# Kernel tuning notes

Hardware: AMD Instinct MI355X
Metric: run time of the kernel (lower is better)

The kernel has to match this reference:

```python
import jax, jax.numpy as jnp
import numpy as np

B, T, F1, F2 = 16384, 5, 300, 251
IN, H = 551, 128

def setup_inputs() -> dict:
    key = jax.random.key(0)
    ks = jax.random.split(key, 16)
    s = 0.05
    return {
        "x1": jax.random.normal(ks[0], (B, T, F1), jnp.float32),
        "x2": jax.random.normal(ks[1], (B, T, F2), jnp.float32),
        "W_ih": jax.random.normal(ks[2], (4 * H, IN), jnp.float32) * s,
        "W_hh": jax.random.normal(ks[3], (4 * H, H), jnp.float32) * s,
        "b_ih": jax.random.normal(ks[4], (4 * H,), jnp.float32) * s,
        "b_hh": jax.random.normal(ks[5], (4 * H,), jnp.float32) * s,
        "W1": jax.random.normal(ks[6], (531, H * T), jnp.float32) * s,
        "b1": jax.random.normal(ks[7], (531,), jnp.float32) * s,
        "W2": jax.random.normal(ks[8], (256, 531), jnp.float32) * s,
        "b2": jax.random.normal(ks[9], (256,), jnp.float32) * s,
        "W3": jax.random.normal(ks[10], (64, 256), jnp.float32) * s,
        "b3": jax.random.normal(ks[11], (64,), jnp.float32) * s,
        "W4": jax.random.normal(ks[12], (2, 64), jnp.float32) * s,
        "b4": jax.random.normal(ks[13], (2,), jnp.float32) * s,
    }

def _lstm(x, W_ih, W_hh, b_ih, b_hh):
    # x: [B, T, IN] -> outputs [B, T, H]; PyTorch gate order i, f, g, o
    xg = jnp.einsum('bti,gi->btg', x, W_ih) + b_ih + b_hh  # [B, T, 4H]
    xg = jnp.transpose(xg, (1, 0, 2))  # [T, B, 4H]
    h0 = jnp.zeros((x.shape[0], H), x.dtype)
    c0 = jnp.zeros((x.shape[0], H), x.dtype)

    def step(carry, xg_t):
        h, c = carry
        g = xg_t + h @ W_hh.T  # [B, 4H]
        i, f, gg, o = jnp.split(g, 4, axis=-1)
        c = jax.nn.sigmoid(f) * c + jax.nn.sigmoid(i) * jnp.tanh(gg)
        h = jax.nn.sigmoid(o) * jnp.tanh(c)
        return (h, c), h

    _, hs = jax.lax.scan(step, (h0, c0), xg)  # hs: [T, B, H]
    return jnp.transpose(hs, (1, 0, 2))

def reference(x1, x2, W_ih, W_hh, b_ih, b_hh, W1, b1, W2, b2, W3, b3, W4, b4):
    x = jnp.concatenate((x1, x2), axis=2)  # [B, T, 551]
    h = _lstm(x, W_ih, W_hh, b_ih, b_hh)   # [B, T, H]
    h = h.reshape(h.shape[0], T * H)
    h = jax.nn.relu(h @ W1.T + b1)
    h = jax.nn.relu(h @ W2.T + b2)
    h = jax.nn.relu(h @ W3.T + b3)
    logits = h @ W4.T + b4
    return jax.nn.softmax(logits, axis=1)
```

## Files before the change

### kernel.cpp

```cpp
#include <hip/hip_runtime.h>
#include <hip/hip_bf16.h>


typedef short  short8  __attribute__((ext_vector_type(8)));
typedef short  short4v __attribute__((ext_vector_type(4)));
typedef float  f32x4   __attribute__((ext_vector_type(4)));

#define MFMA(a, b, c) __builtin_amdgcn_mfma_f32_16x16x32_bf16((a), (b), (c), 0, 0, 0)

__device__ __forceinline__ short f2bs(float f) {
    __hip_bfloat16 h = __float2bfloat16(f);
    union { __hip_bfloat16 h; short s; } u; u.h = h; return u.s;
}
__device__ __forceinline__ float b2f(short s) {
    union { unsigned u; float f; } v; v.u = ((unsigned)(unsigned short)s) << 16; return v.f;
}
__device__ __forceinline__ float sigf(float x)  { return 1.f / (1.f + __expf(-x)); }
__device__ __forceinline__ float mytanh(float x){ return 2.f / (1.f + __expf(-2.f * x)) - 1.f; }

#define BB     16384
#define TT     5
#define F1     300
#define F2     251
#define INF    551
#define KP     576
#define G4     512
#define HH     128
#define FLAT   640
#define L1N    531
#define L1P    576
#define L1KP   544
#define L2N    256
#define L3N    64

#define O_WIH  0u
#define O_WHH  589824u
#define O_W1   720896u
#define O_W2   1458176u
#define O_W3   1736704u
#define O_BG   1769472u
#define O_B1   1771520u
#define O_XG   1773824u
#define O_HS   85659904u
#define WS_NEED 106631424u

__device__ __forceinline__ void pack_b(const float* __restrict__ W, short* __restrict__ dst,
                                       int i, int tpn, int Nsrc, int Ksrc, int ldw)
{
    int tile = i >> 9, rem = i & 511, lane = rem >> 3, jj = rem & 7;
    int tn = tile / tpn, tk = tile - tn * tpn;
    int n = tn * 16 + (lane & 15);
    int k = tk * 32 + (lane >> 4) * 8 + jj;
    float v = (n < Nsrc && k < Ksrc) ? W[n * ldw + k] : 0.f;
    dst[i] = f2bs(v);
}

__global__ void prep_kernel(
    const float* __restrict__ W_ih, const float* __restrict__ W_hh,
    const float* __restrict__ b_ih, const float* __restrict__ b_hh,
    const float* __restrict__ W1,   const float* __restrict__ b1,
    const float* __restrict__ W2,   const float* __restrict__ W3,
    short* __restrict__ Wihp, short* __restrict__ Whhp, float* __restrict__ biasg,
    short* __restrict__ W1p,  float* __restrict__ b1p,  short* __restrict__ W2p,
    short* __restrict__ W3p)
{
    const int N0 = G4 * KP;
    const int N1 = N0 + G4 * HH;
    const int N2 = N1 + L1P * FLAT;
    const int N3 = N2 + L2N * L1KP;
    const int N4 = N3 + L3N * L2N;
    const int N5 = N4 + G4;
    const int N6 = N5 + L1P;
    const int stride = gridDim.x * blockDim.x;
    for (int i = blockIdx.x * blockDim.x + threadIdx.x; i < N6; i += stride) {
        if (i < N0)      pack_b(W_ih, Wihp, i,       18, G4,  INF, INF);
        else if (i < N1) pack_b(W_hh, Whhp, i - N0,   4, G4,  HH,  HH);
        else if (i < N2) pack_b(W1,   W1p,  i - N1,  20, L1N, FLAT, FLAT);
        else if (i < N3) pack_b(W2,   W2p,  i - N2,  17, L2N, L1N, L1N);
        else if (i < N4) pack_b(W3,   W3p,  i - N3,   8, L3N, L2N, L2N);
        else if (i < N5) { int j = i - N4; biasg[j] = b_ih[j] + b_hh[j]; }
        else             { int j = i - N5; b1p[j] = (j < L1N) ? b1[j] : 0.f; }
    }
}

__device__ __forceinline__ float4 ld4(const float* __restrict__ x1r,
                                      const float* __restrict__ x2r, int c)
{
    if (c + 3 < F1) return *(const float4*)(x1r + c);
    if (c + 3 < INF) return *(const float4*)(x2r + (c - F1));
    float4 r;
    r.x = (c + 0 < INF) ? x2r[c - F1 + 0] : 0.f;
    r.y = (c + 1 < INF) ? x2r[c - F1 + 1] : 0.f;
    r.z = (c + 2 < INF) ? x2r[c - F1 + 2] : 0.f;
    r.w = (c + 3 < INF) ? x2r[c - F1 + 3] : 0.f;
    return r;
}

__global__ __launch_bounds__(512, 4) void k1_xgemm(
    const float* __restrict__ x1, const float* __restrict__ x2,
    const short* __restrict__ Wihp, const float* __restrict__ biasg,
    short* __restrict__ xg)
{
    __shared__ __align__(16) short At[2][64][72];
    const int tid  = threadIdx.x;
    const int w    = tid >> 6;
    const int lane = tid & 63;
    const int quad = lane >> 4;
    const int c16  = lane & 15;
    const int m0   = blockIdx.x * 64;
    const int t    = m0 >> 14;
    const int bb   = m0 & 16383;

    const int srow  = tid >> 3;
    const int kslot = tid & 7;
    const float* x1r = x1 + ((size_t)(bb + srow) * TT + t) * F1;
    const float* x2r = x2 + ((size_t)(bb + srow) * TT + t) * F2;

    f32x4 acc[4][4];
#pragma unroll
    for (int mt = 0; mt < 4; ++mt)
#pragma unroll
        for (int nt = 0; nt < 4; ++nt)
            acc[mt][nt] = (f32x4){0.f, 0.f, 0.f, 0.f};

    {
        int c = kslot * 8;
        float4 v0 = *(const float4*)(x1r + c);
        float4 v1 = *(const float4*)(x1r + c + 4);
        short8 s;
        s[0] = f2bs(v0.x); s[1] = f2bs(v0.y); s[2] = f2bs(v0.z); s[3] = f2bs(v0.w);
        s[4] = f2bs(v1.x); s[5] = f2bs(v1.y); s[6] = f2bs(v1.z); s[7] = f2bs(v1.w);
        *(short8*)&At[0][srow][kslot * 8] = s;
    }
    __syncthreads();

    for (int ch = 0; ch < 9; ++ch) {
        const int cur = ch & 1;
        float4 q0, q1;
        if (ch < 8) {
            int c = (ch + 1) * 64 + kslot * 8;
            q0 = ld4(x1r, x2r, c);
            q1 = ld4(x1r, x2r, c + 4);
        }
#pragma unroll
        for (int ks = 0; ks < 2; ++ks) {
            short8 a[4];
#pragma unroll
            for (int mt = 0; mt < 4; ++mt)
                a[mt] = *(const short8*)&At[cur][mt * 16 + c16][ks * 32 + quad * 8];
            const int tk = ch * 2 + ks;
#pragma unroll
            for (int nt = 0; nt < 4; ++nt) {
                short8 b = *(const short8*)&Wihp[(((w * 4 + nt) * 18 + tk) << 9) + lane * 8];
#pragma unroll
                for (int mt = 0; mt < 4; ++mt)
                    acc[mt][nt] = MFMA(a[mt], b, acc[mt][nt]);
            }
        }
        if (ch < 8) {
            short8 s;
            s[0] = f2bs(q0.x); s[1] = f2bs(q0.y); s[2] = f2bs(q0.z); s[3] = f2bs(q0.w);
            s[4] = f2bs(q1.x); s[5] = f2bs(q1.y); s[6] = f2bs(q1.z); s[7] = f2bs(q1.w);
            *(short8*)&At[cur ^ 1][srow][kslot * 8] = s;
        }
        __syncthreads();
    }

#pragma unroll
    for (int nt = 0; nt < 4; ++nt) {
        float bv = biasg[w * 64 + nt * 16 + c16];
#pragma unroll
        for (int mt = 0; mt < 4; ++mt) {
            short4v o;
#pragma unroll
            for (int r = 0; r < 4; ++r) o[r] = f2bs(acc[mt][nt][r] + bv);
            int tm = (m0 >> 4) + mt, tn = w * 4 + nt;
            *(short4v*)&xg[((tm * 32 + tn) << 8) + lane * 4] = o;
        }
    }
}

__global__ __launch_bounds__(512, 2) void k2_rec(
    const short* __restrict__ Whhp, const short* __restrict__ xg,
    short* __restrict__ hs)
{
    __shared__ __align__(16) short hb[2][32][136];
    const int tid  = threadIdx.x;
    const int w    = tid >> 6;
    const int lane = tid & 63;
    const int quad = lane >> 4;
    const int c16  = lane & 15;
    const int btile = blockIdx.x * 2;

    short8 bfr[4][4];
#pragma unroll
    for (int g = 0; g < 4; ++g)
#pragma unroll
        for (int ks = 0; ks < 4; ++ks)
            bfr[g][ks] = *(const short8*)&Whhp[((((g * 8 + w) * 4) + ks) << 9) + lane * 8];

    float cst[2][4];
#pragma unroll
    for (int mt = 0; mt < 2; ++mt)
#pragma unroll
        for (int r = 0; r < 4; ++r) cst[mt][r] = 0.f;

    const int j = w * 16 + c16;

    for (int t = 0; t < TT; ++t) {
        short4v xq[2][4];
#pragma unroll
        for (int mt = 0; mt < 2; ++mt)
#pragma unroll
            for (int g = 0; g < 4; ++g)
                xq[mt][g] = *(const short4v*)
                    &xg[((((t << 10) + btile + mt) * 32 + (g * 8 + w)) << 8) + lane * 4];

        f32x4 acc[2][4];
#pragma unroll
        for (int mt = 0; mt < 2; ++mt)
#pragma unroll
            for (int g = 0; g < 4; ++g)
                acc[mt][g] = (f32x4){0.f, 0.f, 0.f, 0.f};

        if (t > 0) {
            const short (*cur)[136] = hb[(t - 1) & 1];
#pragma unroll
            for (int ks = 0; ks < 4; ++ks) {
                short8 a[2];
#pragma unroll
                for (int mt = 0; mt < 2; ++mt)
                    a[mt] = *(const short8*)&cur[mt * 16 + c16][ks * 32 + quad * 8];
#pragma unroll
                for (int mt = 0; mt < 2; ++mt)
#pragma unroll
                    for (int g = 0; g < 4; ++g)
                        acc[mt][g] = MFMA(a[mt], bfr[g][ks], acc[mt][g]);
            }
        }

        short (*nxt)[136] = hb[t & 1];
#pragma unroll
        for (int mt = 0; mt < 2; ++mt) {
#pragma unroll
            for (int r = 0; r < 4; ++r) {
                int m = mt * 16 + quad * 4 + r;
                float gi = acc[mt][0][r] + b2f(xq[mt][0][r]);
                float gf = acc[mt][1][r] + b2f(xq[mt][1][r]);
                float gg = acc[mt][2][r] + b2f(xq[mt][2][r]);
                float go = acc[mt][3][r] + b2f(xq[mt][3][r]);
                float cn = sigf(gf) * cst[mt][r] + sigf(gi) * mytanh(gg);
                cst[mt][r] = cn;
                nxt[m][j] = f2bs(sigf(go) * mytanh(cn));
            }
        }
        __syncthreads();
        {
            int tm = w >> 2, kt = w & 3;
            short8 v = *(const short8*)&nxt[tm * 16 + c16][kt * 32 + quad * 8];
            *(short8*)&hs[(((btile + tm) * 20 + t * 4 + kt) << 9) + lane * 8] = v;
        }
    }
}

__global__ __launch_bounds__(256, 2) void mlp_kernel(
    const short* __restrict__ hs,
    const short* __restrict__ W1p, const float* __restrict__ b1p,
    const short* __restrict__ W2p, const float* __restrict__ b2,
    const short* __restrict__ W3p, const float* __restrict__ b3,
    const float* __restrict__ W4,  const float* __restrict__ b4,
    float* __restrict__ out)
{
    __shared__ __align__(16) short a1[32][584];
    __shared__ __align__(16) short a2[32][264];
    __shared__ __align__(16) short a3[32][72];
    const int tid  = threadIdx.x;
    const int w    = tid >> 6;
    const int lane = tid & 63;
    const int quad = lane >> 4;
    const int c16  = lane & 15;
    const int m0   = blockIdx.x * 32;
    const int mtile = blockIdx.x * 2;

    {
        f32x4 acc[2][9];
#pragma unroll
        for (int mt = 0; mt < 2; ++mt)
#pragma unroll
            for (int i = 0; i < 9; ++i)
                acc[mt][i] = (f32x4){0.f, 0.f, 0.f, 0.f};
#pragma unroll 4
        for (int ks = 0; ks < 20; ++ks) {
            short8 a[2];
#pragma unroll
            for (int mt = 0; mt < 2; ++mt)
                a[mt] = *(const short8*)&hs[(((mtile + mt) * 20 + ks) << 9) + lane * 8];
#pragma unroll
            for (int i = 0; i < 9; ++i) {
                short8 b = *(const short8*)&W1p[(((w * 9 + i) * 20 + ks) << 9) + lane * 8];
                acc[0][i] = MFMA(a[0], b, acc[0][i]);
                acc[1][i] = MFMA(a[1], b, acc[1][i]);
            }
        }
#pragma unroll
        for (int i = 0; i < 9; ++i) {
            int n = (w * 9 + i) * 16 + c16;
            float bv = b1p[n];
#pragma unroll
            for (int mt = 0; mt < 2; ++mt)
#pragma unroll
                for (int r = 0; r < 4; ++r) {
                    int m = mt * 16 + quad * 4 + r;
                    float v = acc[mt][i][r] + bv;
                    a1[m][n] = f2bs(v > 0.f ? v : 0.f);
                }
        }
    }
    __syncthreads();

    {
        f32x4 acc[2][4];
#pragma unroll
        for (int mt = 0; mt < 2; ++mt)
#pragma unroll
            for (int i = 0; i < 4; ++i)
                acc[mt][i] = (f32x4){0.f, 0.f, 0.f, 0.f};
#pragma unroll 4
        for (int ks = 0; ks < 17; ++ks) {
            short8 a[2];
#pragma unroll
            for (int mt = 0; mt < 2; ++mt)
                a[mt] = *(const short8*)&a1[mt * 16 + c16][ks * 32 + quad * 8];
#pragma unroll
            for (int i = 0; i < 4; ++i) {
                short8 b = *(const short8*)&W2p[(((w * 4 + i) * 17 + ks) << 9) + lane * 8];
                acc[0][i] = MFMA(a[0], b, acc[0][i]);
                acc[1][i] = MFMA(a[1], b, acc[1][i]);
            }
        }
#pragma unroll
        for (int i = 0; i < 4; ++i) {
            int n = (w * 4 + i) * 16 + c16;
            float bv = b2[n];
#pragma unroll
            for (int mt = 0; mt < 2; ++mt)
#pragma unroll
                for (int r = 0; r < 4; ++r) {
                    int m = mt * 16 + quad * 4 + r;
                    float v = acc[mt][i][r] + bv;
                    a2[m][n] = f2bs(v > 0.f ? v : 0.f);
                }
        }
    }
    __syncthreads();

    {
        f32x4 acc[2];
        acc[0] = (f32x4){0.f, 0.f, 0.f, 0.f};
        acc[1] = (f32x4){0.f, 0.f, 0.f, 0.f};
#pragma unroll
        for (int ks = 0; ks < 8; ++ks) {
            short8 a[2];
#pragma unroll
            for (int mt = 0; mt < 2; ++mt)
                a[mt] = *(const short8*)&a2[mt * 16 + c16][ks * 32 + quad * 8];
            short8 b = *(const short8*)&W3p[((w * 8 + ks) << 9) + lane * 8];
            acc[0] = MFMA(a[0], b, acc[0]);
            acc[1] = MFMA(a[1], b, acc[1]);
        }
        int n = w * 16 + c16;
        float bv = b3[n];
#pragma unroll
        for (int mt = 0; mt < 2; ++mt)
#pragma unroll
            for (int r = 0; r < 4; ++r) {
                int m = mt * 16 + quad * 4 + r;
                float v = acc[mt][r] + bv;
                a3[m][n] = f2bs(v > 0.f ? v : 0.f);
            }
    }
    __syncthreads();

    if (tid < 64) {
        int m   = tid >> 1;
        int cls = tid & 1;
        float s = b4[cls];
#pragma unroll 8
        for (int k = 0; k < 64; ++k)
            s += b2f(a3[m][k]) * W4[cls * 64 + k];
        float other = __shfl_xor(s, 1);
        float p = 1.f / (1.f + __expf(other - s));
        out[(m0 + m) * 2 + cls] = p;
    }
}

extern "C" void kernel_launch(void* const* d_in, const int* in_sizes, int n_in,
                              void* d_out, int out_size, void* d_ws, size_t ws_size,
                              hipStream_t stream)
{
    (void)in_sizes; (void)n_in; (void)out_size;
    if (ws_size < (size_t)WS_NEED) return;

    const float* x1   = (const float*)d_in[0];
    const float* x2   = (const float*)d_in[1];
    const float* W_ih = (const float*)d_in[2];
    const float* W_hh = (const float*)d_in[3];
    const float* b_ih = (const float*)d_in[4];
    const float* b_hh = (const float*)d_in[5];
    const float* W1   = (const float*)d_in[6];
    const float* b1   = (const float*)d_in[7];
    const float* W2   = (const float*)d_in[8];
    const float* b2   = (const float*)d_in[9];
    const float* W3   = (const float*)d_in[10];
    const float* b3   = (const float*)d_in[11];
    const float* W4   = (const float*)d_in[12];
    const float* b4   = (const float*)d_in[13];

    char* ws = (char*)d_ws;
    short* Wihp  = (short*)(ws + O_WIH);
    short* Whhp  = (short*)(ws + O_WHH);
    short* W1p   = (short*)(ws + O_W1);
    short* W2p   = (short*)(ws + O_W2);
    short* W3p   = (short*)(ws + O_W3);
    float* biasg = (float*)(ws + O_BG);
    float* b1p   = (float*)(ws + O_B1);
    short* xg    = (short*)(ws + O_XG);
    short* hsb   = (short*)(ws + O_HS);

    prep_kernel<<<3461, 256, 0, stream>>>(W_ih, W_hh, b_ih, b_hh, W1, b1, W2, W3,
                                          Wihp, Whhp, biasg, W1p, b1p, W2p, W3p);
    k1_xgemm<<<1280, 512, 0, stream>>>(x1, x2, Wihp, biasg, xg);
    k2_rec<<<512, 512, 0, stream>>>(Whhp, xg, hsb);
    mlp_kernel<<<512, 256, 0, stream>>>(hsb, W1p, b1p, W2p, b2, W3p, b3, W4, b4,
                                        (float*)d_out);
}
```

Measured before the change: 377.0 us.

## Fuse input GEMM, LSTM recurrence and MLP into one kernel with packed bf16 X

```diff
diff --git a/kernel.cpp b/kernel.cpp
--- a/kernel.cpp
+++ b/kernel.cpp
@@ -7,6 +7,9 @@
 typedef float  f32x4   __attribute__((ext_vector_type(4)));
 
 #define MFMA(a, b, c) __builtin_amdgcn_mfma_f32_16x16x32_bf16((a), (b), (c), 0, 0, 0)
+#define WAITV(N) asm volatile("s_waitcnt vmcnt(" #N ")" ::: "memory")
+#define MEMF()   asm volatile("" ::: "memory")
+#define BAR()    __builtin_amdgcn_s_barrier()
 
 __device__ __forceinline__ short f2bs(float f) {
     __hip_bfloat16 h = __float2bfloat16(f);
@@ -17,6 +20,12 @@
 }
 __device__ __forceinline__ float sigf(float x)  { return 1.f / (1.f + __expf(-x)); }
 __device__ __forceinline__ float mytanh(float x){ return 2.f / (1.f + __expf(-2.f * x)) - 1.f; }
+
+__device__ __forceinline__ void gload16(const short* g, short* l) {
+    __builtin_amdgcn_global_load_lds(
+        (const __attribute__((address_space(1))) void*)g,
+        (__attribute__((address_space(3))) void*)l, 16, 0, 0);
+}
 
 #define BB     16384
 #define TT     5
@@ -40,9 +49,8 @@
 #define O_W3   1736704u
 #define O_BG   1769472u
 #define O_B1   1771520u
-#define O_XG   1773824u
-#define O_HS   85659904u
-#define WS_NEED 106631424u
+#define O_XP   1773824u
+#define WS_NEED 96145664u
 
 __device__ __forceinline__ void pack_b(const float* __restrict__ W, short* __restrict__ dst,
                                        int i, int tpn, int Nsrc, int Ksrc, int ldw)
@@ -83,8 +91,8 @@
     }
 }
 
-__device__ __forceinline__ float4 ld4(const float* __restrict__ x1r,
-                                      const float* __restrict__ x2r, int c)
+__device__ __forceinline__ float4 ld4u(const float* __restrict__ x1r,
+                                       const float* __restrict__ x2r, int c)
 {
     if (c + 3 < F1) return *(const float4*)(x1r + c);
     if (c + 3 < INF) return *(const float4*)(x2r + (c - F1));
@@ -96,101 +104,71 @@
     return r;
 }
 
-__global__ __launch_bounds__(512, 4) void k1_xgemm(
+__global__ __launch_bounds__(256, 4) void packx_kernel(
     const float* __restrict__ x1, const float* __restrict__ x2,
-    const short* __restrict__ Wihp, const float* __restrict__ biasg,
-    short* __restrict__ xg)
-{
-    __shared__ __align__(16) short At[2][64][72];
+    short* __restrict__ Xp)
+{
+    __shared__ __align__(16) short At[16][584];
+    const int tid  = threadIdx.x;
+    const int w    = tid >> 6;
+    const int lane = tid & 63;
+    const int t    = blockIdx.x >> 10;
+    const int bt   = blockIdx.x & 1023;
+    const int b0   = bt << 4;
+
+#pragma unroll
+    for (int rr = 0; rr < 4; ++rr) {
+        int row = w * 4 + rr;
+        const float* x1r = x1 + ((size_t)(b0 + row) * TT + t) * F1;
+        const float* x2r = x2 + ((size_t)(b0 + row) * TT + t) * F2;
+#pragma unroll
+        for (int p = 0; p < 3; ++p) {
+            int c = p * 256 + lane * 4;
+            if (c < 576) {
+                float4 v = ld4u(x1r, x2r, c);
+                short4v s4;
+                s4[0] = f2bs(v.x); s4[1] = f2bs(v.y);
+                s4[2] = f2bs(v.z); s4[3] = f2bs(v.w);
+                *(short4v*)&At[row][c] = s4;
+            }
+        }
+    }
+    __syncthreads();
+
+    const int gm = (t << 10) + bt;
+    for (int slot = tid; slot < 1152; slot += 256) {
+        int tk = slot >> 6, l = slot & 63;
+        short8 v = *(const short8*)&At[l & 15][tk * 32 + ((l >> 4) & 3) * 8];
+        *(short8*)&Xp[((gm * 18 + tk) << 9) + l * 8] = v;
+    }
+}
+
+__global__ __launch_bounds__(512, 2) void fused_kernel(
+    const short* __restrict__ Xp,  const short* __restrict__ Wihp,
+    const short* __restrict__ Whhp, const float* __restrict__ biasg,
+    const short* __restrict__ W1p, const float* __restrict__ b1p,
+    const short* __restrict__ W2p, const float* __restrict__ b2,
+    const short* __restrict__ W3p, const float* __restrict__ b3,
+    const float* __restrict__ W4,  const float* __restrict__ b4,
+    float* __restrict__ out)
+{
+    __shared__ __align__(16) char smem[160768];
+    short*  hsL = (short*)smem;
+    short (*a2)[264] = (short (*)[264])smem;
+    char* R1 = smem + 81920;
+    short (*SA)[4][512]  = (short (*)[4][512])R1;
+    short (*SB)[16][512] = (short (*)[16][512])(R1 + 12288);
+    short (*hb)[136]     = (short (*)[136])(R1 + 61440);
+    short (*a1)[584]     = (short (*)[584])R1;
+    short (*a3)[72]      = (short (*)[72])R1;
+
     const int tid  = threadIdx.x;
     const int w    = tid >> 6;
     const int lane = tid & 63;
     const int quad = lane >> 4;
     const int c16  = lane & 15;
-    const int m0   = blockIdx.x * 64;
-    const int t    = m0 >> 14;
-    const int bb   = m0 & 16383;
-
-    const int srow  = tid >> 3;
-    const int kslot = tid & 7;
-    const float* x1r = x1 + ((size_t)(bb + srow) * TT + t) * F1;
-    const float* x2r = x2 + ((size_t)(bb + srow) * TT + t) * F2;
-
-    f32x4 acc[4][4];
-#pragma unroll
-    for (int mt = 0; mt < 4; ++mt)
-#pragma unroll
-        for (int nt = 0; nt < 4; ++nt)
-            acc[mt][nt] = (f32x4){0.f, 0.f, 0.f, 0.f};
-
-    {
-        int c = kslot * 8;
-        float4 v0 = *(const float4*)(x1r + c);
-        float4 v1 = *(const float4*)(x1r + c + 4);
-        short8 s;
-        s[0] = f2bs(v0.x); s[1] = f2bs(v0.y); s[2] = f2bs(v0.z); s[3] = f2bs(v0.w);
-        s[4] = f2bs(v1.x); s[5] = f2bs(v1.y); s[6] = f2bs(v1.z); s[7] = f2bs(v1.w);
-        *(short8*)&At[0][srow][kslot * 8] = s;
-    }
-    __syncthreads();
-
-    for (int ch = 0; ch < 9; ++ch) {
-        const int cur = ch & 1;
-        float4 q0, q1;
-        if (ch < 8) {
-            int c = (ch + 1) * 64 + kslot * 8;
-            q0 = ld4(x1r, x2r, c);
-            q1 = ld4(x1r, x2r, c + 4);
-        }
-#pragma unroll
-        for (int ks = 0; ks < 2; ++ks) {
-            short8 a[4];
-#pragma unroll
-            for (int mt = 0; mt < 4; ++mt)
-                a[mt] = *(const short8*)&At[cur][mt * 16 + c16][ks * 32 + quad * 8];
-            const int tk = ch * 2 + ks;
-#pragma unroll
-            for (int nt = 0; nt < 4; ++nt) {
-                short8 b = *(const short8*)&Wihp[(((w * 4 + nt) * 18 + tk) << 9) + lane * 8];
-#pragma unroll
-                for (int mt = 0; mt < 4; ++mt)
-                    acc[mt][nt] = MFMA(a[mt], b, acc[mt][nt]);
-            }
-        }
-        if (ch < 8) {
-            short8 s;
-            s[0] = f2bs(q0.x); s[1] = f2bs(q0.y); s[2] = f2bs(q0.z); s[3] = f2bs(q0.w);
-            s[4] = f2bs(q1.x); s[5] = f2bs(q1.y); s[6] = f2bs(q1.z); s[7] = f2bs(q1.w);
-            *(short8*)&At[cur ^ 1][srow][kslot * 8] = s;
-        }
-        __syncthreads();
-    }
-
-#pragma unroll
-    for (int nt = 0; nt < 4; ++nt) {
-        float bv = biasg[w * 64 + nt * 16 + c16];
-#pragma unroll
-        for (int mt = 0; mt < 4; ++mt) {
-            short4v o;
-#pragma unroll
-            for (int r = 0; r < 4; ++r) o[r] = f2bs(acc[mt][nt][r] + bv);
-            int tm = (m0 >> 4) + mt, tn = w * 4 + nt;
-            *(short4v*)&xg[((tm * 32 + tn) << 8) + lane * 4] = o;
-        }
-    }
-}
-
-__global__ __launch_bounds__(512, 2) void k2_rec(
-    const short* __restrict__ Whhp, const short* __restrict__ xg,
-    short* __restrict__ hs)
-{
-    __shared__ __align__(16) short hb[2][32][136];
-    const int tid  = threadIdx.x;
-    const int w    = tid >> 6;
-    const int lane = tid & 63;
-    const int quad = lane >> 4;
-    const int c16  = lane & 15;
-    const int btile = blockIdx.x * 2;
+    const int b0   = blockIdx.x * 64;
+    const int tmb  = blockIdx.x * 4;
 
     short8 bfr[4][4];
 #pragma unroll
@@ -198,162 +176,222 @@
 #pragma unroll
         for (int ks = 0; ks < 4; ++ks)
             bfr[g][ks] = *(const short8*)&Whhp[((((g * 8 + w) * 4) + ks) << 9) + lane * 8];
-
-    float cst[2][4];
-#pragma unroll
-    for (int mt = 0; mt < 2; ++mt)
+    float bv[4];
+#pragma unroll
+    for (int g = 0; g < 4; ++g) bv[g] = biasg[((g * 8 + w) << 4) + c16];
+
+    float cst[4][4];
+#pragma unroll
+    for (int mt = 0; mt < 4; ++mt)
 #pragma unroll
         for (int r = 0; r < 4; ++r) cst[mt][r] = 0.f;
 
-    const int j = w * 16 + c16;
-
     for (int t = 0; t < TT; ++t) {
-        short4v xq[2][4];
-#pragma unroll
-        for (int mt = 0; mt < 2; ++mt)
-#pragma unroll
-            for (int g = 0; g < 4; ++g)
-                xq[mt][g] = *(const short4v*)
-                    &xg[((((t << 10) + btile + mt) * 32 + (g * 8 + w)) << 8) + lane * 4];
-
-        f32x4 acc[2][4];
-#pragma unroll
-        for (int mt = 0; mt < 2; ++mt)
+        f32x4 acc[4][4];
+#pragma unroll
+        for (int mt = 0; mt < 4; ++mt)
 #pragma unroll
             for (int g = 0; g < 4; ++g)
                 acc[mt][g] = (f32x4){0.f, 0.f, 0.f, 0.f};
 
+        auto stageB = [&](int u) {
+            const int tk = u >> 1, p = u & 1;
+#pragma unroll
+            for (int gg = 0; gg < 2; ++gg) {
+                int tn = (2 * p + gg) * 8 + w;
+                gload16(Wihp + ((tn * 18 + tk) << 9) + lane * 8,
+                        &SB[u % 3][gg * 8 + w][lane * 8]);
+            }
+        };
+        auto stageA = [&](int s) {
+            gload16(Xp + ((((t << 10) + tmb + w) * 18 + s) << 9) + lane * 8,
+                    &SA[s % 3][w][lane * 8]);
+        };
+
+        stageB(0);
+        if (w < 4) { stageA(0); stageA(1); }
+        stageB(1);
         if (t > 0) {
-            const short (*cur)[136] = hb[(t - 1) & 1];
 #pragma unroll
             for (int ks = 0; ks < 4; ++ks) {
-                short8 a[2];
-#pragma unroll
-                for (int mt = 0; mt < 2; ++mt)
-                    a[mt] = *(const short8*)&cur[mt * 16 + c16][ks * 32 + quad * 8];
-#pragma unroll
-                for (int mt = 0; mt < 2; ++mt)
-#pragma unroll
-                    for (int g = 0; g < 4; ++g)
-                        acc[mt][g] = MFMA(a[mt], bfr[g][ks], acc[mt][g]);
-            }
-        }
-
-        short (*nxt)[136] = hb[t & 1];
-#pragma unroll
-        for (int mt = 0; mt < 2; ++mt) {
+                short8 ah[4];
+#pragma unroll
+                for (int mt = 0; mt < 4; ++mt)
+                    ah[mt] = *(const short8*)&hb[mt * 16 + c16][ks * 32 + quad * 8];
+#pragma unroll
+                for (int g = 0; g < 4; ++g)
+#pragma unroll
+                    for (int mt = 0; mt < 4; ++mt)
+                        acc[mt][g] = MFMA(ah[mt], bfr[g][ks], acc[mt][g]);
+            }
+        }
+        if (w < 4) { WAITV(3); } else { WAITV(2); }
+        BAR(); MEMF();
+
+#pragma unroll
+        for (int v = 0; v < 32; v += 2) {
+            stageB(v + 2);
+            if (w < 4) stageA(v / 2 + 2);
+            short8 a[4];
+#pragma unroll
+            for (int mt = 0; mt < 4; ++mt)
+                a[mt] = *(const short8*)&SA[(v >> 1) % 3][mt][lane * 8];
+#pragma unroll
+            for (int gg = 0; gg < 2; ++gg) {
+                short8 b = *(const short8*)&SB[v % 3][gg * 8 + w][lane * 8];
+#pragma unroll
+                for (int mt = 0; mt < 4; ++mt)
+                    acc[mt][gg] = MFMA(a[mt], b, acc[mt][gg]);
+            }
+            if (w < 4) { WAITV(3); } else { WAITV(2); }
+            BAR(); MEMF();
+            stageB(v + 3);
+#pragma unroll
+            for (int gg = 0; gg < 2; ++gg) {
+                short8 b = *(const short8*)&SB[(v + 1) % 3][gg * 8 + w][lane * 8];
+#pragma unroll
+                for (int mt = 0; mt < 4; ++mt)
+                    acc[mt][2 + gg] = MFMA(a[mt], b, acc[mt][2 + gg]);
+            }
+            WAITV(2);
+            BAR(); MEMF();
+        }
+        {
+            stageB(34);
+            short8 a[4];
+#pragma unroll
+            for (int mt = 0; mt < 4; ++mt)
+                a[mt] = *(const short8*)&SA[1][mt][lane * 8];
+#pragma unroll
+            for (int gg = 0; gg < 2; ++gg) {
+                short8 b = *(const short8*)&SB[2][gg * 8 + w][lane * 8];
+#pragma unroll
+                for (int mt = 0; mt < 4; ++mt)
+                    acc[mt][gg] = MFMA(a[mt], b, acc[mt][gg]);
+            }
+            WAITV(2); BAR(); MEMF();
+            stageB(35);
+#pragma unroll
+            for (int gg = 0; gg < 2; ++gg) {
+                short8 b = *(const short8*)&SB[0][gg * 8 + w][lane * 8];
+#pragma unroll
+                for (int mt = 0; mt < 4; ++mt)
+                    acc[mt][2 + gg] = MFMA(a[mt], b, acc[mt][2 + gg]);
+            }
+            WAITV(2); BAR(); MEMF();
+            short8 a7[4];
+#pragma unroll
+            for (int mt = 0; mt < 4; ++mt)
+                a7[mt] = *(const short8*)&SA[2][mt][lane * 8];
+#pragma unroll
+            for (int gg = 0; gg < 2; ++gg) {
+                short8 b = *(const short8*)&SB[1][gg * 8 + w][lane * 8];
+#pragma unroll
+                for (int mt = 0; mt < 4; ++mt)
+                    acc[mt][gg] = MFMA(a7[mt], b, acc[mt][gg]);
+            }
+            WAITV(0); BAR(); MEMF();
+#pragma unroll
+            for (int gg = 0; gg < 2; ++gg) {
+                short8 b = *(const short8*)&SB[2][gg * 8 + w][lane * 8];
+#pragma unroll
+                for (int mt = 0; mt < 4; ++mt)
+                    acc[mt][2 + gg] = MFMA(a7[mt], b, acc[mt][2 + gg]);
+            }
+        }
+#pragma unroll
+        for (int mt = 0; mt < 4; ++mt)
 #pragma unroll
             for (int r = 0; r < 4; ++r) {
                 int m = mt * 16 + quad * 4 + r;
-                float gi = acc[mt][0][r] + b2f(xq[mt][0][r]);
-                float gf = acc[mt][1][r] + b2f(xq[mt][1][r]);
-                float gg = acc[mt][2][r] + b2f(xq[mt][2][r]);
-                float go = acc[mt][3][r] + b2f(xq[mt][3][r]);
-                float cn = sigf(gf) * cst[mt][r] + sigf(gi) * mytanh(gg);
+                float gi = acc[mt][0][r] + bv[0];
+                float gf = acc[mt][1][r] + bv[1];
+                float gq = acc[mt][2][r] + bv[2];
+                float go = acc[mt][3][r] + bv[3];
+                float cn = sigf(gf) * cst[mt][r] + sigf(gi) * mytanh(gq);
                 cst[mt][r] = cn;
-                nxt[m][j] = f2bs(sigf(go) * mytanh(cn));
-            }
-        }
+                hb[m][w * 16 + c16] = f2bs(sigf(go) * mytanh(cn));
+            }
         __syncthreads();
-        {
-            int tm = w >> 2, kt = w & 3;
-            short8 v = *(const short8*)&nxt[tm * 16 + c16][kt * 32 + quad * 8];
-            *(short8*)&hs[(((btile + tm) * 20 + t * 4 + kt) << 9) + lane * 8] = v;
-        }
-    }
-}
-
-__global__ __launch_bounds__(256, 2) void mlp_kernel(
-    const short* __restrict__ hs,
-    const short* __restrict__ W1p, const float* __restrict__ b1p,
-    const short* __restrict__ W2p, const float* __restrict__ b2,
-    const short* __restrict__ W3p, const float* __restrict__ b3,
-    const float* __restrict__ W4,  const float* __restrict__ b4,
-    float* __restrict__ out)
-{
-    __shared__ __align__(16) short a1[32][584];
-    __shared__ __align__(16) short a2[32][264];
-    __shared__ __align__(16) short a3[32][72];
-    const int tid  = threadIdx.x;
-    const int w    = tid >> 6;
-    const int lane = tid & 63;
-    const int quad = lane >> 4;
-    const int c16  = lane & 15;
-    const int m0   = blockIdx.x * 32;
-    const int mtile = blockIdx.x * 2;
-
+#pragma unroll
+        for (int i = 0; i < 2; ++i) {
+            int slot = w + 8 * i, tm = slot >> 2, kt = slot & 3;
+            short8 hv = *(const short8*)&hb[tm * 16 + c16][kt * 32 + quad * 8];
+            *(short8*)&hsL[((tm * 20 + (t << 2) + kt) << 9) + lane * 8] = hv;
+        }
+        __syncthreads();
+    }
+
+    const int mh = w >> 2, wn = w & 3;
     {
         f32x4 acc[2][9];
 #pragma unroll
         for (int mt = 0; mt < 2; ++mt)
 #pragma unroll
-            for (int i = 0; i < 9; ++i)
-                acc[mt][i] = (f32x4){0.f, 0.f, 0.f, 0.f};
+            for (int i = 0; i < 9; ++i) acc[mt][i] = (f32x4){0.f, 0.f, 0.f, 0.f};
 #pragma unroll 4
         for (int ks = 0; ks < 20; ++ks) {
             short8 a[2];
 #pragma unroll
             for (int mt = 0; mt < 2; ++mt)
-                a[mt] = *(const short8*)&hs[(((mtile + mt) * 20 + ks) << 9) + lane * 8];
+                a[mt] = *(const short8*)&hsL[(((mh * 2 + mt) * 20 + ks) << 9) + lane * 8];
 #pragma unroll
             for (int i = 0; i < 9; ++i) {
-                short8 b = *(const short8*)&W1p[(((w * 9 + i) * 20 + ks) << 9) + lane * 8];
+                short8 b = *(const short8*)&W1p[(((wn * 9 + i) * 20 + ks) << 9) + lane * 8];
                 acc[0][i] = MFMA(a[0], b, acc[0][i]);
                 acc[1][i] = MFMA(a[1], b, acc[1][i]);
             }
         }
 #pragma unroll
         for (int i = 0; i < 9; ++i) {
-            int n = (w * 9 + i) * 16 + c16;
-            float bv = b1p[n];
+            int n = (wn * 9 + i) * 16 + c16;
+            float bb = b1p[n];
 #pragma unroll
             for (int mt = 0; mt < 2; ++mt)
 #pragma unroll
                 for (int r = 0; r < 4; ++r) {
-                    int m = mt * 16 + quad * 4 + r;
-                    float v = acc[mt][i][r] + bv;
-                    a1[m][n] = f2bs(v > 0.f ? v : 0.f);
+                    int m = (mh * 2 + mt) * 16 + quad * 4 + r;
+                    float vv = acc[mt][i][r] + bb;
+                    a1[m][n] = f2bs(vv > 0.f ? vv : 0.f);
                 }
         }
     }
     __syncthreads();
-
     {
         f32x4 acc[2][4];
 #pragma unroll
         for (int mt = 0; mt < 2; ++mt)
 #pragma unroll
-            for (int i = 0; i < 4; ++i)
-                acc[mt][i] = (f32x4){0.f, 0.f, 0.f, 0.f};
+            for (int i = 0; i < 4; ++i) acc[mt][i] = (f32x4){0.f, 0.f, 0.f, 0.f};
 #pragma unroll 4
         for (int ks = 0; ks < 17; ++ks) {
             short8 a[2];
 #pragma unroll
             for (int mt = 0; mt < 2; ++mt)
-                a[mt] = *(const short8*)&a1[mt * 16 + c16][ks * 32 + quad * 8];
+                a[mt] = *(const short8*)&a1[(mh * 2 + mt) * 16 + c16][ks * 32 + quad * 8];
 #pragma unroll
             for (int i = 0; i < 4; ++i) {
-                short8 b = *(const short8*)&W2p[(((w * 4 + i) * 17 + ks) << 9) + lane * 8];
+                short8 b = *(const short8*)&W2p[(((wn * 4 + i) * 17 + ks) << 9) + lane * 8];
                 acc[0][i] = MFMA(a[0], b, acc[0][i]);
                 acc[1][i] = MFMA(a[1], b, acc[1][i]);
             }
         }
+        __syncthreads();
 #pragma unroll
         for (int i = 0; i < 4; ++i) {
-            int n = (w * 4 + i) * 16 + c16;
-            float bv = b2[n];
+            int n = (wn * 4 + i) * 16 + c16;
+            float bb = b2[n];
 #pragma unroll
             for (int mt = 0; mt < 2; ++mt)
 #pragma unroll
                 for (int r = 0; r < 4; ++r) {
-                    int m = mt * 16 + quad * 4 + r;
-                    float v = acc[mt][i][r] + bv;
-                    a2[m][n] = f2bs(v > 0.f ? v : 0.f);
+                    int m = (mh * 2 + mt) * 16 + quad * 4 + r;
+                    float vv = acc[mt][i][r] + bb;
+                    a2[m][n] = f2bs(vv > 0.f ? vv : 0.f);
                 }
         }
     }
     __syncthreads();
-
     {
         f32x4 acc[2];
         acc[0] = (f32x4){0.f, 0.f, 0.f, 0.f};
@@ -363,34 +401,32 @@
             short8 a[2];
 #pragma unroll
             for (int mt = 0; mt < 2; ++mt)
-                a[mt] = *(const short8*)&a2[mt * 16 + c16][ks * 32 + quad * 8];
-            short8 b = *(const short8*)&W3p[((w * 8 + ks) << 9) + lane * 8];
+                a[mt] = *(const short8*)&a2[(mh * 2 + mt) * 16 + c16][ks * 32 + quad * 8];
+            short8 b = *(const short8*)&W3p[((wn * 8 + ks) << 9) + lane * 8];
             acc[0] = MFMA(a[0], b, acc[0]);
             acc[1] = MFMA(a[1], b, acc[1]);
         }
-        int n = w * 16 + c16;
-        float bv = b3[n];
+        __syncthreads();
+        int n = wn * 16 + c16;
+        float bb = b3[n];
 #pragma unroll
         for (int mt = 0; mt < 2; ++mt)
 #pragma unroll
             for (int r = 0; r < 4; ++r) {
-                int m = mt * 16 + quad * 4 + r;
-                float v = acc[mt][r] + bv;
-                a3[m][n] = f2bs(v > 0.f ? v : 0.f);
+                int m = (mh * 2 + mt) * 16 + quad * 4 + r;
+                float vv = acc[mt][r] + bb;
+                a3[m][n] = f2bs(vv > 0.f ? vv : 0.f);
             }
     }
     __syncthreads();
-
-    if (tid < 64) {
-        int m   = tid >> 1;
-        int cls = tid & 1;
+    if (tid < 128) {
+        int m = tid >> 1, cls = tid & 1;
         float s = b4[cls];
 #pragma unroll 8
         for (int k = 0; k < 64; ++k)
             s += b2f(a3[m][k]) * W4[cls * 64 + k];
         float other = __shfl_xor(s, 1);
-        float p = 1.f / (1.f + __expf(other - s));
-        out[(m0 + m) * 2 + cls] = p;
+        out[(b0 + m) * 2 + cls] = 1.f / (1.f + __expf(other - s));
     }
 }
 
@@ -424,13 +460,12 @@
     short* W3p   = (short*)(ws + O_W3);
     float* biasg = (float*)(ws + O_BG);
     float* b1p   = (float*)(ws + O_B1);
-    short* xg    = (short*)(ws + O_XG);
-    short* hsb   = (short*)(ws + O_HS);
+    short* Xp    = (short*)(ws + O_XP);
 
     prep_kernel<<<3461, 256, 0, stream>>>(W_ih, W_hh, b_ih, b_hh, W1, b1, W2, W3,
                                           Wihp, Whhp, biasg, W1p, b1p, W2p, W3p);
-    k1_xgemm<<<1280, 512, 0, stream>>>(x1, x2, Wihp, biasg, xg);
-    k2_rec<<<512, 512, 0, stream>>>(Whhp, xg, hsb);
-    mlp_kernel<<<512, 256, 0, stream>>>(hsb, W1p, b1p, W2p, b2, W3p, b3, W4, b4,
-                                        (float*)d_out);
-}
+    packx_kernel<<<5120, 256, 0, stream>>>(x1, x2, Xp);
+    fused_kernel<<<256, 512, 0, stream>>>(Xp, Wihp, Whhp, biasg,
+                                          W1p, b1p, W2p, b2, W3p, b3, W4, b4,
+                                          (float*)d_out);
+}
```

After: 486.3 us. +29.0%, slower.
